# Optimization experiments

Measured on AMD Instinct MI355X. Metric: run time of the kernel, lower is better.

The kernel has to match this reference:

```python
import jax, jax.numpy as jnp
import numpy as np

B = 8192      # n_trials
N = 4096      # network size
N_IN = 3      # input channels (1 osc + 2 stim)
TAU = 0.1
DT = 0.0005


def setup_inputs() -> dict:
    key = jax.random.key(0)
    ks = jax.random.split(key, 8)
    k_t = jax.random.normal(ks[0], (B, 2), dtype=jnp.float32)
    phase = jax.random.uniform(ks[1], (B,), dtype=jnp.float32) * 2.0 * np.pi
    monodromy = jnp.tile(jnp.eye(2, dtype=jnp.float32)[None], (B, 1, 1))
    dK_norms = jnp.zeros((B,), dtype=jnp.float32)
    amp = jnp.float32(1.5)
    w = jnp.float32(2.0 * np.pi * 4.0)  # reference oscillation frequency
    stim = jax.random.normal(ks[2], (N_IN - 1,), dtype=jnp.float32)
    alpha = jax.random.normal(ks[3], (2, N_IN), dtype=jnp.float32)
    I = jax.random.normal(ks[4], (N_IN, N), dtype=jnp.float32)
    m = jax.random.normal(ks[5], (2, N), dtype=jnp.float32)
    n = jax.random.normal(ks[6], (2, N), dtype=jnp.float32)
    return {"k_t": k_t, "phase": phase, "monodromy": monodromy,
            "dK_norms": dK_norms, "amp": amp, "w": w, "stim": stim,
            "alpha": alpha, "I": I, "m": m, "n": n}


def reference(k_t, phase, monodromy, dK_norms, amp, w, stim, alpha, I, m, n):
    # calc_x_u
    tau_sw = w * TAU
    v_osc = amp / jnp.sqrt(1.0 + tau_sw ** 2) * jnp.sin(phase - jnp.arctan2(tau_sw, 1.0))  # [B]
    u_osc = amp * jnp.sin(phase)                                                           # [B]
    u_stim = jnp.broadcast_to(stim[None, :], (phase.shape[0], stim.shape[0]))              # [B, n_in-1]
    u = jnp.concatenate([u_osc[:, None], u_stim], axis=-1)                                  # [B, n_in]
    v = jnp.concatenate([v_osc[:, None], u_stim], axis=-1)                                  # [B, n_in]
    x = k_t @ m + v @ I                                                                     # [B, N]
    tx = jnp.tanh(x)
    # dKdt
    dK = (1.0 / TAU) * (-k_t + tx @ n.T / N + u @ alpha.T)                                  # [B, 2]
    # Jacobian: (1/tau) * (-I2 + (1/N) * einsum over neurons)
    dphi = 1.0 - tx ** 2                                                                    # [B, N]
    Jac = (1.0 / TAU) * (-jnp.eye(2, dtype=x.dtype)[None]
                         + jnp.einsum('bn,kn,dn->bkd', dphi, m, n) / N)                     # [B, 2, 2]
    # Euler update
    k_out = k_t + DT * dK
    phase_out = phase + DT * w
    mono_out = monodromy + DT * jnp.einsum('bkd,bde->bke', Jac, monodromy)
    dK_norms_out = dK_norms + jnp.linalg.norm(dK, axis=-1)
    return (k_out, phase_out, mono_out, dK_norms_out)
```

## Files before the change

### kernel.cpp

```cpp
#include <hip/hip_runtime.h>
#include <math.h>

#define N_SIZE 4096
#define B_SIZE 8192
#define NH 2048
#define T_PER_WAVE 2

typedef float v2f __attribute__((ext_vector_type(2)));

__device__ __forceinline__ float wave_sum(float v) {
#pragma unroll
    for (int off = 32; off >= 1; off >>= 1)
        v += __shfl_xor(v, off, 64);
    return v;
}

__device__ __forceinline__ v2f tanh2(v2f x) {
    v2f xe = x * 2.885390081777927f;
    v2f ex;
    ex.x = __builtin_amdgcn_exp2f(xe.x);
    ex.y = __builtin_amdgcn_exp2f(xe.y);
    v2f d = ex + 1.0f;
    v2f r;
    r.x = __builtin_amdgcn_rcpf(d.x);
    r.y = __builtin_amdgcn_rcpf(d.y);
    return 1.0f - 2.0f * r;
}

__global__ __launch_bounds__(512, 4)
void bif_kernel(const float* __restrict__ k_t,
                const float* __restrict__ phase,
                const float* __restrict__ mono,
                const float* __restrict__ dKn,
                const float* __restrict__ amp_p,
                const float* __restrict__ w_p,
                const float* __restrict__ stim,
                const float* __restrict__ alpha,
                const float* __restrict__ Im,
                const float* __restrict__ mm,
                const float* __restrict__ nm,
                float* __restrict__ out) {
    __shared__ float s_m0[NH], s_m1[NH], s_n0[NH], s_n1[NH], s_I0[NH], s_cv[NH];

    const int lane = threadIdx.x & 63;
    const int wid  = threadIdx.x >> 6;
    const int b0   = (blockIdx.x * 8 + wid) * T_PER_WAVE;

    const float amp = amp_p[0];
    const float w   = w_p[0];
    const float st0 = stim[0];
    const float st1 = stim[1];
    const float tau_sw = w * 0.1f;
    const float phi0 = atanf(tau_sw);
    const float vamp = amp / sqrtf(1.0f + tau_sw * tau_sw);

    float k0[T_PER_WAVE], k1[T_PER_WAVE], vo[T_PER_WAVE], uo[T_PER_WAVE], ph[T_PER_WAVE];
#pragma unroll
    for (int t = 0; t < T_PER_WAVE; ++t) {
        int b = b0 + t;
        k0[t] = k_t[2 * b];
        k1[t] = k_t[2 * b + 1];
        float p = phase[b];
        ph[t] = p;
        vo[t] = vamp * sinf(p - phi0);
        uo[t] = amp * sinf(p);
    }

    v2f As0[T_PER_WAVE] = {}, As1[T_PER_WAVE] = {};
    v2f A00[T_PER_WAVE] = {}, A01[T_PER_WAVE] = {};
    v2f A10[T_PER_WAVE] = {}, A11[T_PER_WAVE] = {};

    for (int half = 0; half < 2; ++half) {
        {
            const int t4 = threadIdx.x * 4;
            const int g  = half * NH + t4;
            *(float4*)&s_m0[t4] = *(const float4*)&mm[g];
            *(float4*)&s_m1[t4] = *(const float4*)&mm[N_SIZE + g];
            *(float4*)&s_n0[t4] = *(const float4*)&nm[g];
            *(float4*)&s_n1[t4] = *(const float4*)&nm[N_SIZE + g];
            *(float4*)&s_I0[t4] = *(const float4*)&Im[g];
            float4 i1 = *(const float4*)&Im[N_SIZE + g];
            float4 i2 = *(const float4*)&Im[2 * N_SIZE + g];
            float4 cv;
            cv.x = st0 * i1.x + st1 * i2.x;
            cv.y = st0 * i1.y + st1 * i2.y;
            cv.z = st0 * i1.z + st1 * i2.z;
            cv.w = st0 * i1.w + st1 * i2.w;
            *(float4*)&s_cv[t4] = cv;
        }
        __syncthreads();

#pragma unroll 2
        for (int it = 0; it < NH / 256; ++it) {
            const int j = it * 256 + lane * 4;
            float4 fm0 = *(const float4*)&s_m0[j];
            float4 fm1 = *(const float4*)&s_m1[j];
            float4 fn0 = *(const float4*)&s_n0[j];
            float4 fn1 = *(const float4*)&s_n1[j];
            float4 fi0 = *(const float4*)&s_I0[j];
            float4 fcv = *(const float4*)&s_cv[j];
            v2f Ms0[2] = {{fm0.x, fm0.y}, {fm0.z, fm0.w}};
            v2f Ms1[2] = {{fm1.x, fm1.y}, {fm1.z, fm1.w}};
            v2f Nn0[2] = {{fn0.x, fn0.y}, {fn0.z, fn0.w}};
            v2f Nn1[2] = {{fn1.x, fn1.y}, {fn1.z, fn1.w}};
            v2f Iv[2]  = {{fi0.x, fi0.y}, {fi0.z, fi0.w}};
            v2f Cv[2]  = {{fcv.x, fcv.y}, {fcv.z, fcv.w}};
#pragma unroll
            for (int p = 0; p < 2; ++p) {
#pragma unroll
                for (int t = 0; t < T_PER_WAVE; ++t) {
                    v2f x  = Cv[p] + k0[t] * Ms0[p] + k1[t] * Ms1[p] + vo[t] * Iv[p];
                    v2f tx = tanh2(x);
                    v2f dphi = 1.0f - tx * tx;
                    v2f a0 = dphi * Ms0[p];
                    v2f a1 = dphi * Ms1[p];
                    As0[t] += tx * Nn0[p];
                    As1[t] += tx * Nn1[p];
                    A00[t] += a0 * Nn0[p];
                    A01[t] += a0 * Nn1[p];
                    A10[t] += a1 * Nn0[p];
                    A11[t] += a1 * Nn1[p];
                }
            }
        }
        __syncthreads();
    }

    const float a00 = alpha[0], a01 = alpha[1], a02 = alpha[2];
    const float a10 = alpha[3], a11 = alpha[4], a12 = alpha[5];
    const float invN = 1.0f / 4096.0f;
    const float DT = 0.0005f;
#pragma unroll
    for (int t = 0; t < T_PER_WAVE; ++t) {
        float s0  = wave_sum(As0[t].x + As0[t].y);
        float s1  = wave_sum(As1[t].x + As1[t].y);
        float j00 = wave_sum(A00[t].x + A00[t].y);
        float j01 = wave_sum(A01[t].x + A01[t].y);
        float j10 = wave_sum(A10[t].x + A10[t].y);
        float j11 = wave_sum(A11[t].x + A11[t].y);
        if (lane == 0) {
            const int b = b0 + t;
            float ua0 = uo[t] * a00 + st0 * a01 + st1 * a02;
            float ua1 = uo[t] * a10 + st0 * a11 + st1 * a12;
            float dK0 = 10.0f * (-k0[t] + s0 * invN + ua0);
            float dK1 = 10.0f * (-k1[t] + s1 * invN + ua1);
            out[2 * b]     = fmaf(DT, dK0, k0[t]);
            out[2 * b + 1] = fmaf(DT, dK1, k1[t]);
            out[B_SIZE * 2 + b] = ph[t] + DT * w;
            float J00 = 10.0f * (j00 * invN - 1.0f);
            float J01 = 10.0f * (j01 * invN);
            float J10 = 10.0f * (j10 * invN);
            float J11 = 10.0f * (j11 * invN - 1.0f);
            float M00 = mono[4 * b], M01 = mono[4 * b + 1];
            float M10 = mono[4 * b + 2], M11 = mono[4 * b + 3];
            float* om = out + B_SIZE * 3 + 4 * b;
            om[0] = M00 + DT * (J00 * M00 + J01 * M10);
            om[1] = M01 + DT * (J00 * M01 + J01 * M11);
            om[2] = M10 + DT * (J10 * M00 + J11 * M10);
            om[3] = M11 + DT * (J10 * M01 + J11 * M11);
            out[B_SIZE * 7 + b] = dKn[b] + sqrtf(dK0 * dK0 + dK1 * dK1);
        }
    }
}

extern "C" void kernel_launch(void* const* d_in, const int* in_sizes, int n_in,
                              void* d_out, int out_size, void* d_ws, size_t ws_size,
                              hipStream_t stream) {
    const float* k_t   = (const float*)d_in[0];
    const float* phase = (const float*)d_in[1];
    const float* mono  = (const float*)d_in[2];
    const float* dKn   = (const float*)d_in[3];
    const float* amp   = (const float*)d_in[4];
    const float* w     = (const float*)d_in[5];
    const float* stim  = (const float*)d_in[6];
    const float* alpha = (const float*)d_in[7];
    const float* Im    = (const float*)d_in[8];
    const float* mm    = (const float*)d_in[9];
    const float* nm    = (const float*)d_in[10];
    float* out = (float*)d_out;

    bif_kernel<<<B_SIZE / (8 * T_PER_WAVE), 512, 0, stream>>>(
        k_t, phase, mono, dKn, amp, w, stim, alpha, Im, mm, nm, out);
}
```

Measured before the change: 25.15 us.

## Split neuron dimension across wave pairs with 4 trials per wave and 1024-thread blocks

Blocks grow to 1024 threads and stage all 4096 neuron parameters in LDS once, which removes the two-phase reload and the sync between halves. Each pair of waves handles the same 4 trials, one wave per neuron half, and the two partial sums are combined through shared memory. Each wave now carries 4 trials instead of 2, so every LDS vector read is reused twice as much. The costs are higher register pressure from 4 trials of accumulators, 96KB of LDS per block that limits blocks per CU, and a smaller grid of 256 blocks.

```diff
diff --git a/kernel.cpp b/kernel.cpp
--- a/kernel.cpp
+++ b/kernel.cpp
@@ -3,8 +3,8 @@
 
 #define N_SIZE 4096
 #define B_SIZE 8192
-#define NH 2048
-#define T_PER_WAVE 2
+#define T 4
+#define NHALF 2048
 
 typedef float v2f __attribute__((ext_vector_type(2)));
 
@@ -27,7 +27,7 @@
     return 1.0f - 2.0f * r;
 }
 
-__global__ __launch_bounds__(512, 4)
+__global__ __launch_bounds__(1024)
 void bif_kernel(const float* __restrict__ k_t,
                 const float* __restrict__ phase,
                 const float* __restrict__ mono,
@@ -40,126 +40,149 @@
                 const float* __restrict__ mm,
                 const float* __restrict__ nm,
                 float* __restrict__ out) {
-    __shared__ float s_m0[NH], s_m1[NH], s_n0[NH], s_n1[NH], s_I0[NH], s_cv[NH];
-
-    const int lane = threadIdx.x & 63;
-    const int wid  = threadIdx.x >> 6;
-    const int b0   = (blockIdx.x * 8 + wid) * T_PER_WAVE;
+    __shared__ float s_m0[N_SIZE], s_m1[N_SIZE], s_n0[N_SIZE], s_n1[N_SIZE];
+    __shared__ float s_I0[N_SIZE], s_cv[N_SIZE];
+    __shared__ float s_red[8 * 2 * 6 * T];
+
+    const int tid  = threadIdx.x;
+    const int lane = tid & 63;
+    const int wvi  = tid >> 6;
+    const int g    = wvi >> 1;
+    const int h    = wvi & 1;
+    const int b0   = blockIdx.x * 32 + g * T;
+
+    const float st0 = stim[0];
+    const float st1 = stim[1];
+
+    {
+        const int t4 = tid * 4;
+        *(float4*)&s_m0[t4] = *(const float4*)&mm[t4];
+        *(float4*)&s_m1[t4] = *(const float4*)&mm[N_SIZE + t4];
+        *(float4*)&s_n0[t4] = *(const float4*)&nm[t4];
+        *(float4*)&s_n1[t4] = *(const float4*)&nm[N_SIZE + t4];
+        *(float4*)&s_I0[t4] = *(const float4*)&Im[t4];
+        float4 i1 = *(const float4*)&Im[N_SIZE + t4];
+        float4 i2 = *(const float4*)&Im[2 * N_SIZE + t4];
+        float4 cv;
+        cv.x = st0 * i1.x + st1 * i2.x;
+        cv.y = st0 * i1.y + st1 * i2.y;
+        cv.z = st0 * i1.z + st1 * i2.z;
+        cv.w = st0 * i1.w + st1 * i2.w;
+        *(float4*)&s_cv[t4] = cv;
+    }
 
     const float amp = amp_p[0];
     const float w   = w_p[0];
-    const float st0 = stim[0];
-    const float st1 = stim[1];
     const float tau_sw = w * 0.1f;
     const float phi0 = atanf(tau_sw);
     const float vamp = amp / sqrtf(1.0f + tau_sw * tau_sw);
 
-    float k0[T_PER_WAVE], k1[T_PER_WAVE], vo[T_PER_WAVE], uo[T_PER_WAVE], ph[T_PER_WAVE];
-#pragma unroll
-    for (int t = 0; t < T_PER_WAVE; ++t) {
-        int b = b0 + t;
+    float k0[T], k1[T], vo[T];
+#pragma unroll
+    for (int t = 0; t < T; ++t) {
+        const int b = b0 + t;
         k0[t] = k_t[2 * b];
         k1[t] = k_t[2 * b + 1];
-        float p = phase[b];
-        ph[t] = p;
-        vo[t] = vamp * sinf(p - phi0);
-        uo[t] = amp * sinf(p);
-    }
-
-    v2f As0[T_PER_WAVE] = {}, As1[T_PER_WAVE] = {};
-    v2f A00[T_PER_WAVE] = {}, A01[T_PER_WAVE] = {};
-    v2f A10[T_PER_WAVE] = {}, A11[T_PER_WAVE] = {};
-
-    for (int half = 0; half < 2; ++half) {
-        {
-            const int t4 = threadIdx.x * 4;
-            const int g  = half * NH + t4;
-            *(float4*)&s_m0[t4] = *(const float4*)&mm[g];
-            *(float4*)&s_m1[t4] = *(const float4*)&mm[N_SIZE + g];
-            *(float4*)&s_n0[t4] = *(const float4*)&nm[g];
-            *(float4*)&s_n1[t4] = *(const float4*)&nm[N_SIZE + g];
-            *(float4*)&s_I0[t4] = *(const float4*)&Im[g];
-            float4 i1 = *(const float4*)&Im[N_SIZE + g];
-            float4 i2 = *(const float4*)&Im[2 * N_SIZE + g];
-            float4 cv;
-            cv.x = st0 * i1.x + st1 * i2.x;
-            cv.y = st0 * i1.y + st1 * i2.y;
-            cv.z = st0 * i1.z + st1 * i2.z;
-            cv.w = st0 * i1.w + st1 * i2.w;
-            *(float4*)&s_cv[t4] = cv;
-        }
-        __syncthreads();
-
+        vo[t] = vamp * sinf(phase[b] - phi0);
+    }
+
+    __syncthreads();
+
+    v2f As0[T] = {}, As1[T] = {};
+    v2f A00[T] = {}, A01[T] = {};
+    v2f A10[T] = {}, A11[T] = {};
+
+    const int base = h * NHALF;
 #pragma unroll 2
-        for (int it = 0; it < NH / 256; ++it) {
-            const int j = it * 256 + lane * 4;
-            float4 fm0 = *(const float4*)&s_m0[j];
-            float4 fm1 = *(const float4*)&s_m1[j];
-            float4 fn0 = *(const float4*)&s_n0[j];
-            float4 fn1 = *(const float4*)&s_n1[j];
-            float4 fi0 = *(const float4*)&s_I0[j];
-            float4 fcv = *(const float4*)&s_cv[j];
-            v2f Ms0[2] = {{fm0.x, fm0.y}, {fm0.z, fm0.w}};
-            v2f Ms1[2] = {{fm1.x, fm1.y}, {fm1.z, fm1.w}};
-            v2f Nn0[2] = {{fn0.x, fn0.y}, {fn0.z, fn0.w}};
-            v2f Nn1[2] = {{fn1.x, fn1.y}, {fn1.z, fn1.w}};
-            v2f Iv[2]  = {{fi0.x, fi0.y}, {fi0.z, fi0.w}};
-            v2f Cv[2]  = {{fcv.x, fcv.y}, {fcv.z, fcv.w}};
-#pragma unroll
-            for (int p = 0; p < 2; ++p) {
-#pragma unroll
-                for (int t = 0; t < T_PER_WAVE; ++t) {
-                    v2f x  = Cv[p] + k0[t] * Ms0[p] + k1[t] * Ms1[p] + vo[t] * Iv[p];
-                    v2f tx = tanh2(x);
-                    v2f dphi = 1.0f - tx * tx;
-                    v2f a0 = dphi * Ms0[p];
-                    v2f a1 = dphi * Ms1[p];
-                    As0[t] += tx * Nn0[p];
-                    As1[t] += tx * Nn1[p];
-                    A00[t] += a0 * Nn0[p];
-                    A01[t] += a0 * Nn1[p];
-                    A10[t] += a1 * Nn0[p];
-                    A11[t] += a1 * Nn1[p];
-                }
+    for (int it = 0; it < NHALF / 256; ++it) {
+        const int j = base + it * 256 + lane * 4;
+        float4 fm0 = *(const float4*)&s_m0[j];
+        float4 fm1 = *(const float4*)&s_m1[j];
+        float4 fn0 = *(const float4*)&s_n0[j];
+        float4 fn1 = *(const float4*)&s_n1[j];
+        float4 fi0 = *(const float4*)&s_I0[j];
+        float4 fcv = *(const float4*)&s_cv[j];
+        v2f Ms0[2] = {{fm0.x, fm0.y}, {fm0.z, fm0.w}};
+        v2f Ms1[2] = {{fm1.x, fm1.y}, {fm1.z, fm1.w}};
+        v2f Nn0[2] = {{fn0.x, fn0.y}, {fn0.z, fn0.w}};
+        v2f Nn1[2] = {{fn1.x, fn1.y}, {fn1.z, fn1.w}};
+        v2f Iv[2]  = {{fi0.x, fi0.y}, {fi0.z, fi0.w}};
+        v2f Cv[2]  = {{fcv.x, fcv.y}, {fcv.z, fcv.w}};
+#pragma unroll
+        for (int p = 0; p < 2; ++p) {
+#pragma unroll
+            for (int t = 0; t < T; ++t) {
+                v2f x  = Cv[p] + k0[t] * Ms0[p] + k1[t] * Ms1[p] + vo[t] * Iv[p];
+                v2f tx = tanh2(x);
+                v2f dphi = 1.0f - tx * tx;
+                v2f a0 = dphi * Ms0[p];
+                v2f a1 = dphi * Ms1[p];
+                As0[t] += tx * Nn0[p];
+                As1[t] += tx * Nn1[p];
+                A00[t] += a0 * Nn0[p];
+                A01[t] += a0 * Nn1[p];
+                A10[t] += a1 * Nn0[p];
+                A11[t] += a1 * Nn1[p];
             }
         }
-        __syncthreads();
-    }
-
-    const float a00 = alpha[0], a01 = alpha[1], a02 = alpha[2];
-    const float a10 = alpha[3], a11 = alpha[4], a12 = alpha[5];
-    const float invN = 1.0f / 4096.0f;
-    const float DT = 0.0005f;
-#pragma unroll
-    for (int t = 0; t < T_PER_WAVE; ++t) {
-        float s0  = wave_sum(As0[t].x + As0[t].y);
-        float s1  = wave_sum(As1[t].x + As1[t].y);
-        float j00 = wave_sum(A00[t].x + A00[t].y);
-        float j01 = wave_sum(A01[t].x + A01[t].y);
-        float j10 = wave_sum(A10[t].x + A10[t].y);
-        float j11 = wave_sum(A11[t].x + A11[t].y);
+    }
+
+#pragma unroll
+    for (int t = 0; t < T; ++t) {
+        float r0 = wave_sum(As0[t].x + As0[t].y);
+        float r1 = wave_sum(As1[t].x + As1[t].y);
+        float r2 = wave_sum(A00[t].x + A00[t].y);
+        float r3 = wave_sum(A01[t].x + A01[t].y);
+        float r4 = wave_sum(A10[t].x + A10[t].y);
+        float r5 = wave_sum(A11[t].x + A11[t].y);
         if (lane == 0) {
-            const int b = b0 + t;
-            float ua0 = uo[t] * a00 + st0 * a01 + st1 * a02;
-            float ua1 = uo[t] * a10 + st0 * a11 + st1 * a12;
-            float dK0 = 10.0f * (-k0[t] + s0 * invN + ua0);
-            float dK1 = 10.0f * (-k1[t] + s1 * invN + ua1);
-            out[2 * b]     = fmaf(DT, dK0, k0[t]);
-            out[2 * b + 1] = fmaf(DT, dK1, k1[t]);
-            out[B_SIZE * 2 + b] = ph[t] + DT * w;
-            float J00 = 10.0f * (j00 * invN - 1.0f);
-            float J01 = 10.0f * (j01 * invN);
-            float J10 = 10.0f * (j10 * invN);
-            float J11 = 10.0f * (j11 * invN - 1.0f);
-            float M00 = mono[4 * b], M01 = mono[4 * b + 1];
-            float M10 = mono[4 * b + 2], M11 = mono[4 * b + 3];
-            float* om = out + B_SIZE * 3 + 4 * b;
-            om[0] = M00 + DT * (J00 * M00 + J01 * M10);
-            om[1] = M01 + DT * (J00 * M01 + J01 * M11);
-            om[2] = M10 + DT * (J10 * M00 + J11 * M10);
-            om[3] = M11 + DT * (J10 * M01 + J11 * M11);
-            out[B_SIZE * 7 + b] = dKn[b] + sqrtf(dK0 * dK0 + dK1 * dK1);
+            float* rp = &s_red[((g * 2 + h) * 6) * T + t];
+            rp[0 * T] = r0; rp[1 * T] = r1; rp[2 * T] = r2;
+            rp[3 * T] = r3; rp[4 * T] = r4; rp[5 * T] = r5;
         }
+    }
+    __syncthreads();
+
+    if (h == 0 && lane < T) {
+        const int t = lane;
+        const int b = b0 + t;
+        const float* r0p = &s_red[((g * 2 + 0) * 6) * T + t];
+        const float* r1p = &s_red[((g * 2 + 1) * 6) * T + t];
+        float s0  = r0p[0 * T] + r1p[0 * T];
+        float s1  = r0p[1 * T] + r1p[1 * T];
+        float j00 = r0p[2 * T] + r1p[2 * T];
+        float j01 = r0p[3 * T] + r1p[3 * T];
+        float j10 = r0p[4 * T] + r1p[4 * T];
+        float j11 = r0p[5 * T] + r1p[5 * T];
+
+        const float kk0 = k_t[2 * b];
+        const float kk1 = k_t[2 * b + 1];
+        const float p   = phase[b];
+        const float uo  = amp * sinf(p);
+        const float a00 = alpha[0], a01 = alpha[1], a02 = alpha[2];
+        const float a10 = alpha[3], a11 = alpha[4], a12 = alpha[5];
+        const float invN = 1.0f / 4096.0f;
+        const float DT = 0.0005f;
+
+        float ua0 = uo * a00 + st0 * a01 + st1 * a02;
+        float ua1 = uo * a10 + st0 * a11 + st1 * a12;
+        float dK0 = 10.0f * (-kk0 + s0 * invN + ua0);
+        float dK1 = 10.0f * (-kk1 + s1 * invN + ua1);
+        out[2 * b]     = fmaf(DT, dK0, kk0);
+        out[2 * b + 1] = fmaf(DT, dK1, kk1);
+        out[B_SIZE * 2 + b] = p + DT * w;
+        float J00 = 10.0f * (j00 * invN - 1.0f);
+        float J01 = 10.0f * (j01 * invN);
+        float J10 = 10.0f * (j10 * invN);
+        float J11 = 10.0f * (j11 * invN - 1.0f);
+        float M00 = mono[4 * b], M01 = mono[4 * b + 1];
+        float M10 = mono[4 * b + 2], M11 = mono[4 * b + 3];
+        float* om = out + B_SIZE * 3 + 4 * b;
+        om[0] = M00 + DT * (J00 * M00 + J01 * M10);
+        om[1] = M01 + DT * (J00 * M01 + J01 * M11);
+        om[2] = M10 + DT * (J10 * M00 + J11 * M10);
+        om[3] = M11 + DT * (J10 * M01 + J11 * M11);
+        out[B_SIZE * 7 + b] = dKn[b] + sqrtf(dK0 * dK0 + dK1 * dK1);
     }
 }
 
@@ -179,6 +202,6 @@
     const float* nm    = (const float*)d_in[10];
     float* out = (float*)d_out;
 
-    bif_kernel<<<B_SIZE / (8 * T_PER_WAVE), 512, 0, stream>>>(
+    bif_kernel<<<B_SIZE / 32, 1024, 0, stream>>>(
         k_t, phase, mono, dKn, amp, w, stim, alpha, Im, mm, nm, out);
 }
```

New measurement: 24.73 us. About the same (-1.6%).
